# Kernel optimization log

Measured on AMD Instinct MI355X. Metric: run time of the kernel, lower is better.

The kernel has to match this reference:

```python
import jax, jax.numpy as jnp
import numpy as np

N = 20000   # nodes per type (lnc and dis)
E = 160000  # edges per meta-path graph and per pos/neg link graph
H = 8       # attention heads
D = 32      # out_size per head (H*D = 256 flattened)
HID = 256   # hidden_size from ResNet projection


def _bn(x, g, b, eps=1e-5):
    # training-mode BatchNorm1d (biased variance, like torch)
    m = x.mean(0)
    v = x.var(0)
    return g * (x - m) * jax.lax.rsqrt(v + eps) + b


def _leaky(x, slope):
    return jnp.where(x >= 0, x, slope * x)


def _gat(h_src, h_dst, src, dst, W, al, ar, n_dst):
    # DGL GATConv (bipartite, shared fc, no bias, eval mode)
    fs = (h_src @ W).reshape(-1, H, D)          # [Ns,H,D]
    fd = (h_dst @ W).reshape(-1, H, D)          # [Nd,H,D]
    el = (fs * al).sum(-1)                      # [Ns,H]
    er = (fd * ar).sum(-1)                      # [Nd,H]
    e = _leaky(el[src] + er[dst], 0.2)          # [E,H]
    emax = jax.ops.segment_max(e, dst, num_segments=n_dst)
    emax = jnp.where(jnp.isfinite(emax), emax, 0.0)   # zero in-degree safety
    ee = jnp.exp(e - emax[dst])
    den = jax.ops.segment_sum(ee, dst, num_segments=n_dst)
    a = ee / jnp.maximum(den[dst], 1e-9)        # edge softmax over incoming edges
    out = jax.ops.segment_sum(a[:, :, None] * fs[src], dst, num_segments=n_dst)
    return _leaky(out, 0.01).reshape(n_dst, H * D)  # activation=F.leaky_relu, flatten(1)


def _sem_attn(z, W1, b1, w2):
    # z: [N, 2, H*D]; SemanticAttention
    w = (jnp.tanh(z @ W1 + b1) @ w2).mean(0)    # [2]
    beta = jax.nn.softmax(w, axis=0)            # [2]
    return (beta[None, :, None] * z).sum(1)     # [N, H*D]


def setup_inputs() -> dict:
    key = jax.random.key(0)
    ks = jax.random.split(key, 32)
    s = 0.05
    inp = {
        "x_lnc": jax.random.normal(ks[0], (N, 256), jnp.float32),
        "x_dis": jax.random.normal(ks[1], (N, 256), jnp.float32),
        "proj_W": jax.random.normal(ks[2], (2, 256, HID), jnp.float32) * s,
        "proj_bn_g": jnp.ones((HID,), jnp.float32),
        "proj_bn_b": jnp.zeros((HID,), jnp.float32),
        "short_W": jax.random.normal(ks[3], (2, 256, HID), jnp.float32) * s,
        "short_b": jnp.zeros((2, HID), jnp.float32),
        "gat_W": jax.random.normal(ks[4], (4, HID, H * D), jnp.float32) * s,
        "gat_al": jax.random.normal(ks[5], (4, H, D), jnp.float32) * s,
        "gat_ar": jax.random.normal(ks[6], (4, H, D), jnp.float32) * s,
        "sem_W1": jax.random.normal(ks[7], (H * D, 128), jnp.float32) * s,
        "sem_b1": jnp.zeros((128,), jnp.float32),
        "sem_w2": jax.random.normal(ks[8], (128,), jnp.float32) * s,
    }
    names = ["ld_src", "ld_dst", "ll_src", "ll_dst", "dl_src", "dl_dst",
             "dd_src", "dd_dst", "pos_src", "pos_dst", "neg_src", "neg_dst"]
    for i, nm in enumerate(names):
        inp[nm] = jax.random.randint(ks[10 + i], (E,), 0, N, jnp.int32)
    return inp


def reference(x_lnc, x_dis, proj_W, proj_bn_g, proj_bn_b, short_W, short_b,
              gat_W, gat_al, gat_ar, sem_W1, sem_b1, sem_w2,
              ld_src, ld_dst, ll_src, ll_dst, dl_src, dl_dst,
              dd_src, dd_dst, pos_src, pos_dst, neg_src, neg_dst):
    # ResNet projection (shared BN applied per-branch, training-mode stats)
    l_x = _leaky(_bn(x_lnc @ proj_W[0], proj_bn_g, proj_bn_b), 0.01) + (x_lnc @ short_W[0] + short_b[0])
    d_x = _leaky(_bn(x_dis @ proj_W[1], proj_bn_g, proj_bn_b), 0.01) + (x_dis @ short_W[1] + short_b[1])
    # HANLayer: 4 meta-path GATs with pairings (l,d),(l,l),(d,l),(d,d)
    e0 = _gat(l_x, d_x, ld_src, ld_dst, gat_W[0], gat_al[0], gat_ar[0], N)  # dst dis
    e1 = _gat(l_x, l_x, ll_src, ll_dst, gat_W[1], gat_al[1], gat_ar[1], N)  # dst lnc
    e2 = _gat(d_x, l_x, dl_src, dl_dst, gat_W[2], gat_al[2], gat_ar[2], N)  # dst lnc
    e3 = _gat(d_x, d_x, dd_src, dd_dst, gat_W[3], gat_al[3], gat_ar[3], N)  # dst dis
    l_embs = _sem_attn(jnp.stack((e1, e2), axis=1), sem_W1, sem_b1, sem_w2)
    d_embs = _sem_attn(jnp.stack((e0, e3), axis=1), sem_W1, sem_b1, sem_w2)
    # Hadamard u_mul_v over 'lnc-dis' edges (pos graph and neg graph)
    pos_z = l_embs[pos_src] * d_embs[pos_dst]
    neg_z = l_embs[neg_src] * d_embs[neg_dst]
    return pos_z, neg_z, l_embs, d_embs
```

## Files before the change

### kernel.cpp

```cpp
#include <hip/hip_runtime.h>
#include <math.h>

#define NN 20000
#define NE 160000
#define SLOT 40

typedef _Float16 f16;
typedef __attribute__((ext_vector_type(8))) _Float16 f16x8;
typedef __attribute__((ext_vector_type(4))) float f32x4;

__device__ __forceinline__ float leakyf(float x, float s){ return x >= 0.f ? x : s*x; }
__device__ __forceinline__ ushort f2h(float x){ f16 h = (f16)x; ushort u; __builtin_memcpy(&u,&h,2); return u; }
__device__ __forceinline__ float h2f(ushort u){ f16 h; __builtin_memcpy(&h,&u,2); return (float)h; }

__device__ __forceinline__ void gload_lds16(const void* g, void* l){
  __builtin_amdgcn_global_load_lds((const __attribute__((address_space(1))) uint*)g,
                                   (__attribute__((address_space(3))) uint*)l, 16, 0, 0);
}
__device__ __forceinline__ void nts4(float* p, f32x4 v){
  __builtin_nontemporal_store(v, (f32x4*)p);
}

__global__ __launch_bounds__(256) void prep(const float* __restrict__ x_lnc,
    const float* __restrict__ x_dis, const float* __restrict__ proj_W,
    const float* __restrict__ short_W, const float* __restrict__ gat_W,
    const float* __restrict__ gat_al, const float* __restrict__ gat_ar,
    const float* __restrict__ sem_W1,
    ushort* __restrict__ xhl, ushort* __restrict__ xhd,
    ushort* btpl, ushort* btpd, ushort* btgl, ushort* btgd, ushort* btsm,
    int* __restrict__ zbuf){
  int b = blockIdx.x;
  if (b < 10000){
    const float* in = (b >= 5000) ? x_dis : x_lnc;
    ushort* out = (b >= 5000) ? xhd : xhl;
    long idx = (long)(b % 5000)*256 + threadIdx.x;
    long r = idx>>6; int c4 = (int)(idx&63)<<2;
    float4 v = *(const float4*)(in + r*256 + c4);
    ushort4 o; o.x=f2h(v.x); o.y=f2h(v.y); o.z=f2h(v.z); o.w=f2h(v.w);
    *(ushort4*)(out + r*256 + c4) = o;
  } else if (b < 10168){
    int t = b - 10000;
    const float* S; ushort* outb; int n0, k0, ldS=256, colbase;
    if (t < 160){
      int m = t >> 4, tt = t & 15;
      n0 = (tt & 3) * 64; k0 = (tt >> 2) * 64;
      switch(m){
        case 0: S=proj_W;        outb=btpl; colbase=0;   break;
        case 1: S=short_W;       outb=btpl; colbase=256; break;
        case 2: S=proj_W+65536;  outb=btpd; colbase=0;   break;
        case 3: S=short_W+65536; outb=btpd; colbase=256; break;
        case 4: S=gat_W;         outb=btgl; colbase=0;   break;
        case 5: S=gat_W+65536;   outb=btgl; colbase=256; break;
        case 6: S=gat_W+131072;  outb=btgl; colbase=512; break;
        case 7: S=gat_W;         outb=btgd; colbase=0;   break;
        case 8: S=gat_W+131072;  outb=btgd; colbase=256; break;
        default:S=gat_W+196608;  outb=btgd; colbase=512; break;
      }
    } else {
      int s = t - 160;
      n0 = (s & 1)*64; k0 = (s >> 1)*64; ldS = 128;
      S = sem_W1; outb = btsm; colbase = 0;
    }
    __shared__ float tile[64][65];
    int tr = threadIdx.x >> 6;
    int tc = threadIdx.x & 63;
    #pragma unroll
    for (int p=0;p<16;p++){
      int kr = p*4 + tr;
      tile[kr][tc] = S[(size_t)(k0+kr)*ldS + n0 + tc];
    }
    __syncthreads();
    #pragma unroll
    for (int p=0;p<16;p++){
      int nr = p*4 + tr;
      outb[(size_t)(colbase + n0 + nr)*256 + k0 + tc] = f2h(tile[tc][nr]);
    }
  } else if (b < 10232){
    int idx = (b-10168)*256 + threadIdx.x;
    int side = idx >> 13;
    int r = idx & 8191;
    int c = r >> 8;
    int k = r & 255;
    int h = c & 7, sel = c >> 3;
    int gi; const float* av;
    if (side==0){
      gi = (sel==0)?0:((sel==3)?2:1);
      av = (sel<=1)? gat_al : gat_ar;
    } else {
      gi = (sel==0)?0:((sel==1)?2:3);
      av = (sel==1||sel==2)? gat_al : gat_ar;
    }
    const float* wrow = gat_W + gi*65536 + (size_t)k*256 + h*32;
    const float* a = av + gi*256 + h*32;
    float s = 0.f;
    #pragma unroll
    for (int d=0; d<32; d++) s += wrow[d]*a[d];
    ushort* out = side ? btgd : btgl;
    out[(size_t)(768+c)*256 + k] = f2h(s);
  } else if (b < 10328){
    int idx = (b-10232)*256 + threadIdx.x;
    uint* pl = (uint*)(btgl + 800*256);
    uint* pd = (uint*)(btgd + 800*256);
    if (idx < 12288) pl[idx] = 0; else pd[idx-12288] = 0;
  } else {
    int idx = (b-10328)*256 + threadIdx.x;
    if (idx < 81028) zbuf[idx] = 0;
  }
}

template<int EPI>
__global__ __launch_bounds__(256) void gemm16(
    const ushort* __restrict__ A0, const ushort* __restrict__ A1,
    const ushort* __restrict__ B0, const ushort* __restrict__ B1,
    ushort* __restrict__ C0, ushort* __restrict__ C1, int ldc, int M,
    float* __restrict__ sbuf,
    float* __restrict__ elr_l, float* __restrict__ elr_d,
    const float* __restrict__ b1v, const float* __restrict__ w2v,
    const int* s0, const int* s1, const int* s2, const int* s3,
    const int* d0, const int* d1, const int* d2, const int* d3,
    int* __restrict__ cnt, int* __restrict__ slots){
  const int z = blockIdx.z;
  if (EPI==1 && z==2){
    int bb = blockIdx.y*gridDim.x + blockIdx.x;
    int tid = bb*256 + (int)threadIdx.x;
    if (tid < NE){
      #pragma unroll
      for (int g=0; g<4; g++){
        const int* src = (g==0)?s0:(g==1)?s1:(g==2)?s2:s3;
        const int* dst = (g==0)?d0:(g==1)?d1:(g==2)?d2:d3;
        int d = dst[tid];
        int p = atomicAdd(&cnt[g*NN + d], 1);
        slots[(size_t)(g*NN + d)*SLOT + p] = src[tid];
      }
    }
    return;
  }
  int bx, by;
  {
    int gx = gridDim.x, gy = gridDim.y;
    int nwg = gx*gy;
    int bid = blockIdx.y*gx + blockIdx.x;
    int q = nwg>>3, r = nwg&7;
    int xcd = bid&7, ii = bid>>3;
    int swz = (xcd<r ? xcd*(q+1) : r*(q+1)+(xcd-r)*q) + ii;
    bx = swz % gx; by = swz / gx;
  }
  const ushort* A = z ? A1 : A0;
  const ushort* Bt = z ? B1 : B0;
  ushort* C = z ? C1 : C0;
  __shared__ ushort sm[16384];
  char* smc = (char*)sm;
  const int tid = threadIdx.x;
  const int lane = tid & 63, wid = tid >> 6;
  const int wr = wid >> 1, wc = wid & 1;
  const int fr = lane & 15, fq = lane >> 4;
  const int brow = by*128, bcol = bx*128;
  f32x4 acc[4][4];
  #pragma unroll
  for (int i=0;i<4;i++)
    #pragma unroll
    for (int j=0;j<4;j++) acc[i][j] = (f32x4){0.f,0.f,0.f,0.f};

  for (int k0 = 0; k0 < 256; k0 += 64){
    __syncthreads();
    #pragma unroll
    for (int cc = 0; cc < 8; cc++){
      int c = wid*8 + cc;
      int ch = c & 15;
      int rel = ch*1024 + lane*16;
      int row = rel >> 7;
      int scb = (rel & 127) ^ ((row & 7) << 4);
      const char* src;
      if (c < 16){
        int gr = brow + row; gr = (gr < M) ? gr : (M-1);
        src = (const char*)A + (size_t)gr*512 + k0*2 + scb;
      } else {
        src = (const char*)Bt + (size_t)(bcol + row)*512 + k0*2 + scb;
      }
      gload_lds16(src, smc + ((c<16)?0:16384) + ch*1024);
    }
    __syncthreads();
    #pragma unroll
    for (int ks = 0; ks < 2; ks++){
      f16x8 af[4], bfr[4];
      #pragma unroll
      for (int i=0;i<4;i++){
        int r = wr*64 + i*16 + fr;
        int koff = ks*32 + fq*8;
        int aoff = ((r<<7) + koff*2) ^ ((r&7)<<4);
        af[i] = *(const f16x8*)(smc + aoff);
        int n = wc*64 + i*16 + fr;
        int boff = ((n<<7) + koff*2) ^ ((n&7)<<4);
        bfr[i] = *(const f16x8*)(smc + 16384 + boff);
      }
      #pragma unroll
      for (int i=0;i<4;i++)
        #pragma unroll
        for (int j=0;j<4;j++)
          acc[i][j] = __builtin_amdgcn_mfma_f32_16x16x32_f16(af[i], bfr[j], acc[i][j], 0,0,0);
    }
  }

  if (EPI==1 || (EPI==2 && bcol < 768)){
    #pragma unroll
    for (int i=0;i<4;i++){
      #pragma unroll
      for (int e=0;e<4;e++){
        int gr = brow + wr*64 + i*16 + fq*4 + e;
        if (gr < M){
          #pragma unroll
          for (int j=0;j<4;j++)
            C[(size_t)gr*ldc + bcol + wc*64 + j*16 + fr] = f2h(acc[i][j][e]);
        }
      }
    }
  }

  if (EPI==2 && bcol >= 768 && wc == 0){
    float* elr = z ? elr_d : elr_l;
    #pragma unroll
    for (int i=0;i<4;i++){
      #pragma unroll
      for (int e=0;e<4;e++){
        int gr = brow + wr*64 + i*16 + fq*4 + e;
        if (gr < M){
          elr[(size_t)gr*32 + fr]      = acc[i][0][e];
          elr[(size_t)gr*32 + 16 + fr] = acc[i][1][e];
        }
      }
    }
  }

  if (EPI==1 && bcol < 256){
    float* gsum = sbuf + z*512;
    float* gsq  = gsum + 256;
    #pragma unroll
    for (int j=0;j<4;j++){
      float s=0.f, q=0.f;
      #pragma unroll
      for (int i=0;i<4;i++)
        #pragma unroll
        for (int e=0;e<4;e++){
          int gr = brow + wr*64 + i*16 + fq*4 + e;
          if (gr < M){ float v = acc[i][j][e]; s += v; q += v*v; }
        }
      s += __shfl_xor(s,16); s += __shfl_xor(s,32);
      q += __shfl_xor(q,16); q += __shfl_xor(q,32);
      if (fq==0){
        int gc = bcol + wc*64 + j*16 + fr;
        atomicAdd(&gsum[gc], s);
        atomicAdd(&gsq[gc], q);
      }
    }
  }

  if (EPI==3){
    float b1c[4], w2c[4];
    #pragma unroll
    for (int j=0;j<4;j++){
      int col = wc*64 + j*16 + fr;
      b1c[j] = b1v[col]; w2c[j] = w2v[col];
    }
    int segA = brow/20000;
    int bound = (segA+1)*20000;
    float t0=0.f, t1=0.f;
    #pragma unroll
    for (int i=0;i<4;i++){
      #pragma unroll
      for (int e=0;e<4;e++){
        int gr = brow + wr*64 + i*16 + fq*4 + e;
        float rs = 0.f;
        #pragma unroll
        for (int j=0;j<4;j++){
          float x = acc[i][j][e] + b1c[j];
          float ex = __expf(2.f*x);
          rs += (1.f - 2.f/(ex+1.f))*w2c[j];
        }
        if (gr < bound) t0 += rs; else t1 += rs;
      }
    }
    #pragma unroll
    for (int off=32; off>0; off>>=1){ t0 += __shfl_xor(t0,off); t1 += __shfl_xor(t1,off); }
    if (lane==0){
      atomicAdd(&sbuf[segA], t0);
      if (brow + 127 >= bound) atomicAdd(&sbuf[segA+1], t1);
    }
  }
}

__global__ __launch_bounds__(256) void proj_apply2(const ushort* __restrict__ PS_l,
    const ushort* __restrict__ PS_d, const float* __restrict__ sbuf,
    const float* __restrict__ gg, const float* __restrict__ bb,
    const float* __restrict__ short_b, ushort* __restrict__ out_l, ushort* __restrict__ out_d){
  int y = blockIdx.y;
  const ushort* PS = y ? PS_d : PS_l;
  ushort* out = y ? out_d : out_l;
  const float* gsum = sbuf + y*512;
  const float* gsq  = gsum + 256;
  const float* sb = short_b + y*256;
  long idx = (long)blockIdx.x*256 + threadIdx.x;
  long r = idx>>6; int c4 = (int)(idx&63)<<2;
  ushort4 pu = *(const ushort4*)(PS + r*512 + c4);
  ushort4 su = *(const ushort4*)(PS + r*512 + 256 + c4);
  float pv[4] = {h2f(pu.x),h2f(pu.y),h2f(pu.z),h2f(pu.w)};
  float sv[4] = {h2f(su.x),h2f(su.y),h2f(su.z),h2f(su.w)};
  ushort o[4];
  #pragma unroll
  for (int k=0;k<4;k++){
    int c = c4+k;
    float m = gsum[c]*(1.f/NN);
    float va = gsq[c]*(1.f/NN) - m*m;
    float ri = rsqrtf(va + 1e-5f);
    float yv = (pv[k]-m)*ri*gg[c] + bb[c];
    o[k] = f2h(leakyf(yv,0.01f) + sv[k] + sb[c]);
  }
  ushort4 ov; ov.x=o[0]; ov.y=o[1]; ov.z=o[2]; ov.w=o[3];
  *(ushort4*)(out + r*256 + c4) = ov;
}

__global__ __launch_bounds__(256) void gat_fused(const int* __restrict__ cnt,
    const int* __restrict__ slots, const float* __restrict__ elr_l,
    const float* __restrict__ elr_d, const ushort* __restrict__ fc_l,
    const ushort* __restrict__ fc_d, ushort* __restrict__ sems){
  const int g = blockIdx.y;
  const int n = blockIdx.x*4 + (threadIdx.x>>6);
  const int lane = threadIdx.x & 63;
  const int co[4]    = {0,256,256,512};
  const int semo[4]  = {40000,0,20000,60000};
  const int eloA[4]  = {0,8,8,16};
  const int eroA[4]  = {0,16,24,24};
  const float* elb = (g<2) ? elr_l : elr_d;
  const float* erb = (g==1||g==2) ? elr_l : elr_d;
  const int eloff = eloA[g], eroff = eroA[g];
  const ushort* F = (g<2) ? fc_l : fc_d;
  const int coloff = co[g];
  const int j = lane>>3, h = lane&7, hc = lane>>3;
  const int e1 = cnt[g*NN + n];
  const long sb = (long)(g*NN + n)*SLOT;
  const float ern = erb[(size_t)n*32 + eroff + h];
  float ssum = 0.f;
  float4 acc = make_float4(0.f,0.f,0.f,0.f);

  for (int base = 0; base < e1; base += 8){
    int idx = base + j;
    bool valid = idx < e1;
    int src = valid ? slots[sb + idx] : 0;
    float p = valid ? __expf(leakyf(elb[(size_t)src*32 + eloff + h] + ern, 0.2f)) : 0.f;
    ssum += p;
    #pragma unroll
    for (int e=0;e<8;e++){
      float w = __shfl(p, e*8 + hc);
      int s = __shfl(src, e*8);
      ushort4 fu = *(const ushort4*)(F + (size_t)s*768 + coloff + lane*4);
      acc.x = fmaf(w,h2f(fu.x),acc.x); acc.y = fmaf(w,h2f(fu.y),acc.y);
      acc.z = fmaf(w,h2f(fu.z),acc.z); acc.w = fmaf(w,h2f(fu.w),acc.w);
    }
  }
  ssum += __shfl_xor(ssum,8); ssum += __shfl_xor(ssum,16); ssum += __shfl_xor(ssum,32);
  float rd = 1.f/fmaxf(__shfl(ssum, hc), 1e-9f);
  ushort4 o;
  o.x = f2h(leakyf(acc.x*rd, 0.01f)); o.y = f2h(leakyf(acc.y*rd, 0.01f));
  o.z = f2h(leakyf(acc.z*rd, 0.01f)); o.w = f2h(leakyf(acc.w*rd, 0.01f));
  *(ushort4*)(sems + (size_t)(semo[g]+n)*256 + lane*4) = o;
}

__global__ __launch_bounds__(256) void sem_combine(const ushort* __restrict__ sems,
    const float* __restrict__ tsum, float* __restrict__ lemb, float* __restrict__ demb,
    ushort* __restrict__ lemb16, ushort* __restrict__ demb16){
  float wl0 = tsum[0]*(1.f/20000.f), wl1 = tsum[1]*(1.f/20000.f);
  float m = fmaxf(wl0,wl1);
  float ea = __expf(wl0-m), eb = __expf(wl1-m);
  float b0 = ea/(ea+eb), b1 = eb/(ea+eb);
  float wd0 = tsum[2]*(1.f/20000.f), wd1 = tsum[3]*(1.f/20000.f);
  m = fmaxf(wd0,wd1);
  ea = __expf(wd0-m); eb = __expf(wd1-m);
  float b2 = ea/(ea+eb), b3 = eb/(ea+eb);

  long idx = (long)blockIdx.x*256 + threadIdx.x;
  long r = idx>>6; int c4 = (int)(idx&63)<<2;
  ushort4 v1 = *(const ushort4*)(sems + (r          )*256 + c4);
  ushort4 v2 = *(const ushort4*)(sems + (r + 20000L )*256 + c4);
  ushort4 v0 = *(const ushort4*)(sems + (r + 40000L )*256 + c4);
  ushort4 v3 = *(const ushort4*)(sems + (r + 60000L )*256 + c4);
  f32x4 lo, dd;
  lo[0] = b0*h2f(v1.x) + b1*h2f(v2.x); dd[0] = b2*h2f(v0.x) + b3*h2f(v3.x);
  lo[1] = b0*h2f(v1.y) + b1*h2f(v2.y); dd[1] = b2*h2f(v0.y) + b3*h2f(v3.y);
  lo[2] = b0*h2f(v1.z) + b1*h2f(v2.z); dd[2] = b2*h2f(v0.z) + b3*h2f(v3.z);
  lo[3] = b0*h2f(v1.w) + b1*h2f(v2.w); dd[3] = b2*h2f(v0.w) + b3*h2f(v3.w);
  nts4(lemb + r*256 + c4, lo);
  nts4(demb + r*256 + c4, dd);
  ushort4 lh, dh;
  lh.x=f2h(lo[0]); lh.y=f2h(lo[1]); lh.z=f2h(lo[2]); lh.w=f2h(lo[3]);
  dh.x=f2h(dd[0]); dh.y=f2h(dd[1]); dh.z=f2h(dd[2]); dh.w=f2h(dd[3]);
  *(ushort4*)(lemb16 + r*256 + c4) = lh;
  *(ushort4*)(demb16 + r*256 + c4) = dh;
}

__global__ __launch_bounds__(256) void edge_mul2(const int* __restrict__ ps, const int* __restrict__ pd,
    const int* __restrict__ ns, const int* __restrict__ nd,
    const ushort* __restrict__ lemb16, const ushort* __restrict__ demb16,
    float* __restrict__ pos, float* __restrict__ neg){
  long idx = (long)blockIdx.x*256 + threadIdx.x;
  const long H = (long)NE*32;
  const int *es, *ed; float* out; long t;
  if (idx < H){ es=ps; ed=pd; out=pos; t=idx; }
  else { es=ns; ed=nd; out=neg; t=idx-H; }
  long i = t>>5; int jj = (int)(t&31);
  int s = es[i], d = ed[i];
  f16x8 a = *(const f16x8*)(lemb16 + (size_t)s*256 + (size_t)jj*8);
  f16x8 b = *(const f16x8*)(demb16 + (size_t)d*256 + (size_t)jj*8);
  f32x4 o0, o1;
  o0[0]=(float)a[0]*(float)b[0]; o0[1]=(float)a[1]*(float)b[1];
  o0[2]=(float)a[2]*(float)b[2]; o0[3]=(float)a[3]*(float)b[3];
  o1[0]=(float)a[4]*(float)b[4]; o1[1]=(float)a[5]*(float)b[5];
  o1[2]=(float)a[6]*(float)b[6]; o1[3]=(float)a[7]*(float)b[7];
  float* op = out + (size_t)i*256 + (size_t)jj*8;
  nts4(op, o0);
  nts4(op+4, o1);
}

extern "C" void kernel_launch(void* const* d_in, const int* in_sizes, int n_in,
                              void* d_out, int out_size, void* d_ws, size_t ws_size,
                              hipStream_t stream){
  const float* x_lnc  = (const float*)d_in[0];
  const float* x_dis  = (const float*)d_in[1];
  const float* proj_W = (const float*)d_in[2];
  const float* bn_g   = (const float*)d_in[3];
  const float* bn_b   = (const float*)d_in[4];
  const float* short_W= (const float*)d_in[5];
  const float* short_b= (const float*)d_in[6];
  const float* gat_W  = (const float*)d_in[7];
  const float* gat_al = (const float*)d_in[8];
  const float* gat_ar = (const float*)d_in[9];
  const float* sem_W1 = (const float*)d_in[10];
  const float* sem_b1 = (const float*)d_in[11];
  const float* sem_w2 = (const float*)d_in[12];
  const int* g_src[4] = {(const int*)d_in[13],(const int*)d_in[15],(const int*)d_in[17],(const int*)d_in[19]};
  const int* g_dst[4] = {(const int*)d_in[14],(const int*)d_in[16],(const int*)d_in[18],(const int*)d_in[20]};
  const int* pos_src = (const int*)d_in[21];
  const int* pos_dst = (const int*)d_in[22];
  const int* neg_src = (const int*)d_in[23];
  const int* neg_dst = (const int*)d_in[24];

  const long LEMB = (long)NN*256;
  const long EOUT = (long)NE*256;

  float* outf = (float*)d_out;
  float* pos  = outf;
  float* negr = outf + EOUT;
  float* lemb = outf + 2*EOUT;
  float* demb = lemb + LEMB;

  ushort* PS_l = (ushort*)negr;
  ushort* PS_d = PS_l + 10240000;
  ushort* fc_l = (ushort*)negr;
  ushort* fc_d = fc_l + 15360000;

  float* ws   = (float*)d_ws;
  float* sbuf = ws;
  float* tsum = ws + 1024;
  int*   cnt  = (int*)(ws + 1028);
  float* elr_l = ws + 81028;
  float* elr_d = elr_l + 640000;
  int*   slots  = (int*)(elr_d + 640000);
  ushort* xhl  = (ushort*)(slots + 3200000);
  ushort* xhd  = xhl + 5120000;
  ushort* axl  = xhd + 5120000;
  ushort* axd  = axl + 5120000;
  ushort* sems = axd + 5120000;
  ushort* lemb16 = sems + 20480000;
  ushort* demb16 = lemb16 + 5120000;
  ushort* btpl = demb16 + 5120000;
  ushort* btpd = btpl + 131072;
  ushort* btgl = btpd + 131072;
  ushort* btgd = btgl + 229376;
  ushort* btsm = btgd + 229376;

  prep<<<10645,256,0,stream>>>(x_lnc, x_dis, proj_W, short_W, gat_W, gat_al, gat_ar,
                               sem_W1, xhl, xhd, btpl, btpd, btgl, btgd, btsm, (int*)ws);

  gemm16<1><<<dim3(4,157,3),256,0,stream>>>(xhl, xhd, btpl, btpd, PS_l, PS_d, 512, NN,
      sbuf, nullptr, nullptr, nullptr, nullptr,
      g_src[0],g_src[1],g_src[2],g_src[3], g_dst[0],g_dst[1],g_dst[2],g_dst[3],
      cnt, slots);
  proj_apply2<<<dim3(5000,2),256,0,stream>>>(PS_l, PS_d, sbuf, bn_g, bn_b, short_b, axl, axd);

  gemm16<2><<<dim3(7,157,2),256,0,stream>>>(axl, axd, btgl, btgd, fc_l, fc_d, 768, NN,
      nullptr, elr_l, elr_d, nullptr, nullptr,
      nullptr,nullptr,nullptr,nullptr, nullptr,nullptr,nullptr,nullptr, nullptr,nullptr);

  gat_fused<<<dim3(5000,4),256,0,stream>>>(cnt, slots, elr_l, elr_d, fc_l, fc_d, sems);

  gemm16<3><<<dim3(1,625,1),256,0,stream>>>(sems, nullptr, btsm, nullptr, nullptr, nullptr, 128, 80000,
      tsum, nullptr, nullptr, sem_b1, sem_w2,
      nullptr,nullptr,nullptr,nullptr, nullptr,nullptr,nullptr,nullptr, nullptr,nullptr);

  sem_combine<<<5000,256,0,stream>>>(sems, tsum, lemb, demb, lemb16, demb16);

  edge_mul2<<<40000,256,0,stream>>>(pos_src, pos_dst, neg_src, neg_dst, lemb16, demb16, pos, negr);
}
```

Before: 364.1 us.

## Fuse fp32-to-fp16 input conversion into projection GEMM A-tile loads

Removes the separate conversion pass in prep that wrote fp16 copies of x_lnc and x_dis. The EPI==1 GEMM now reads fp32 rows directly, converts them to fp16 in registers and writes the swizzled tile into LDS. This saves a full read/write round trip of both inputs and shrinks the prep launch. It also drops the XCD-aware block swizzle for all GEMMs, which may change L2 locality, and replaces the async global_load_lds path for A with ordinary loads and LDS stores that read twice as many bytes.

```diff
diff --git a/kernel.cpp b/kernel.cpp
--- a/kernel.cpp
+++ b/kernel.cpp
@@ -21,25 +21,15 @@
   __builtin_nontemporal_store(v, (f32x4*)p);
 }
 
-__global__ __launch_bounds__(256) void prep(const float* __restrict__ x_lnc,
-    const float* __restrict__ x_dis, const float* __restrict__ proj_W,
+__global__ __launch_bounds__(256) void prep(const float* __restrict__ proj_W,
     const float* __restrict__ short_W, const float* __restrict__ gat_W,
     const float* __restrict__ gat_al, const float* __restrict__ gat_ar,
     const float* __restrict__ sem_W1,
-    ushort* __restrict__ xhl, ushort* __restrict__ xhd,
     ushort* btpl, ushort* btpd, ushort* btgl, ushort* btgd, ushort* btsm,
     int* __restrict__ zbuf){
   int b = blockIdx.x;
-  if (b < 10000){
-    const float* in = (b >= 5000) ? x_dis : x_lnc;
-    ushort* out = (b >= 5000) ? xhd : xhl;
-    long idx = (long)(b % 5000)*256 + threadIdx.x;
-    long r = idx>>6; int c4 = (int)(idx&63)<<2;
-    float4 v = *(const float4*)(in + r*256 + c4);
-    ushort4 o; o.x=f2h(v.x); o.y=f2h(v.y); o.z=f2h(v.z); o.w=f2h(v.w);
-    *(ushort4*)(out + r*256 + c4) = o;
-  } else if (b < 10168){
-    int t = b - 10000;
+  if (b < 168){
+    int t = b;
     const float* S; ushort* outb; int n0, k0, ldS=256, colbase;
     if (t < 160){
       int m = t >> 4, tt = t & 15;
@@ -75,8 +65,8 @@
       int nr = p*4 + tr;
       outb[(size_t)(colbase + n0 + nr)*256 + k0 + tc] = f2h(tile[tc][nr]);
     }
-  } else if (b < 10232){
-    int idx = (b-10168)*256 + threadIdx.x;
+  } else if (b < 232){
+    int idx = (b-168)*256 + threadIdx.x;
     int side = idx >> 13;
     int r = idx & 8191;
     int c = r >> 8;
@@ -97,19 +87,20 @@
     for (int d=0; d<32; d++) s += wrow[d]*a[d];
     ushort* out = side ? btgd : btgl;
     out[(size_t)(768+c)*256 + k] = f2h(s);
-  } else if (b < 10328){
-    int idx = (b-10232)*256 + threadIdx.x;
+  } else if (b < 328){
+    int idx = (b-232)*256 + threadIdx.x;
     uint* pl = (uint*)(btgl + 800*256);
     uint* pd = (uint*)(btgd + 800*256);
     if (idx < 12288) pl[idx] = 0; else pd[idx-12288] = 0;
   } else {
-    int idx = (b-10328)*256 + threadIdx.x;
+    int idx = (b-328)*256 + threadIdx.x;
     if (idx < 81028) zbuf[idx] = 0;
   }
 }
 
 template<int EPI>
 __global__ __launch_bounds__(256) void gemm16(
+    const float* __restrict__ Af0, const float* __restrict__ Af1,
     const ushort* __restrict__ A0, const ushort* __restrict__ A1,
     const ushort* __restrict__ B0, const ushort* __restrict__ B1,
     ushort* __restrict__ C0, ushort* __restrict__ C1, int ldc, int M,
@@ -135,16 +126,7 @@
     }
     return;
   }
-  int bx, by;
-  {
-    int gx = gridDim.x, gy = gridDim.y;
-    int nwg = gx*gy;
-    int bid = blockIdx.y*gx + blockIdx.x;
-    int q = nwg>>3, r = nwg&7;
-    int xcd = bid&7, ii = bid>>3;
-    int swz = (xcd<r ? xcd*(q+1) : r*(q+1)+(xcd-r)*q) + ii;
-    bx = swz % gx; by = swz / gx;
-  }
+  const float* Af = z ? Af1 : Af0;
   const ushort* A = z ? A1 : A0;
   const ushort* Bt = z ? B1 : B0;
   ushort* C = z ? C1 : C0;
@@ -154,7 +136,7 @@
   const int lane = tid & 63, wid = tid >> 6;
   const int wr = wid >> 1, wc = wid & 1;
   const int fr = lane & 15, fq = lane >> 4;
-  const int brow = by*128, bcol = bx*128;
+  const int brow = blockIdx.y*128, bcol = blockIdx.x*128;
   f32x4 acc[4][4];
   #pragma unroll
   for (int i=0;i<4;i++)
@@ -169,15 +151,26 @@
       int ch = c & 15;
       int rel = ch*1024 + lane*16;
       int row = rel >> 7;
-      int scb = (rel & 127) ^ ((row & 7) << 4);
-      const char* src;
+      int colb = rel & 127;
+      int scb = colb ^ ((row & 7) << 4);
       if (c < 16){
         int gr = brow + row; gr = (gr < M) ? gr : (M-1);
-        src = (const char*)A + (size_t)gr*512 + k0*2 + scb;
+        if (EPI==1){
+          const float* srcf = Af + (size_t)gr*256 + k0 + (colb>>1);
+          float4 v0 = *(const float4*)(srcf);
+          float4 v1 = *(const float4*)(srcf + 4);
+          f16x8 hv;
+          hv[0]=(f16)v0.x; hv[1]=(f16)v0.y; hv[2]=(f16)v0.z; hv[3]=(f16)v0.w;
+          hv[4]=(f16)v1.x; hv[5]=(f16)v1.y; hv[6]=(f16)v1.z; hv[7]=(f16)v1.w;
+          *(f16x8*)(smc + (rel & ~127) + scb) = hv;
+        } else {
+          const char* src = (const char*)A + (size_t)gr*512 + k0*2 + scb;
+          gload_lds16(src, smc + ch*1024);
+        }
       } else {
-        src = (const char*)Bt + (size_t)(bcol + row)*512 + k0*2 + scb;
-      }
-      gload_lds16(src, smc + ((c<16)?0:16384) + ch*1024);
+        const char* src = (const char*)Bt + (size_t)(bcol + row)*512 + k0*2 + scb;
+        gload_lds16(src, smc + 16384 + ch*1024);
+      }
     }
     __syncthreads();
     #pragma unroll
@@ -463,9 +456,7 @@
   float* elr_l = ws + 81028;
   float* elr_d = elr_l + 640000;
   int*   slots  = (int*)(elr_d + 640000);
-  ushort* xhl  = (ushort*)(slots + 3200000);
-  ushort* xhd  = xhl + 5120000;
-  ushort* axl  = xhd + 5120000;
+  ushort* axl  = (ushort*)(slots + 3200000);
   ushort* axd  = axl + 5120000;
   ushort* sems = axd + 5120000;
   ushort* lemb16 = sems + 20480000;
@@ -476,22 +467,25 @@
   ushort* btgd = btgl + 229376;
   ushort* btsm = btgd + 229376;
 
-  prep<<<10645,256,0,stream>>>(x_lnc, x_dis, proj_W, short_W, gat_W, gat_al, gat_ar,
-                               sem_W1, xhl, xhd, btpl, btpd, btgl, btgd, btsm, (int*)ws);
-
-  gemm16<1><<<dim3(4,157,3),256,0,stream>>>(xhl, xhd, btpl, btpd, PS_l, PS_d, 512, NN,
+  prep<<<645,256,0,stream>>>(proj_W, short_W, gat_W, gat_al, gat_ar,
+                             sem_W1, btpl, btpd, btgl, btgd, btsm, (int*)ws);
+
+  gemm16<1><<<dim3(4,157,3),256,0,stream>>>(x_lnc, x_dis, nullptr, nullptr,
+      btpl, btpd, PS_l, PS_d, 512, NN,
       sbuf, nullptr, nullptr, nullptr, nullptr,
       g_src[0],g_src[1],g_src[2],g_src[3], g_dst[0],g_dst[1],g_dst[2],g_dst[3],
       cnt, slots);
   proj_apply2<<<dim3(5000,2),256,0,stream>>>(PS_l, PS_d, sbuf, bn_g, bn_b, short_b, axl, axd);
 
-  gemm16<2><<<dim3(7,157,2),256,0,stream>>>(axl, axd, btgl, btgd, fc_l, fc_d, 768, NN,
+  gemm16<2><<<dim3(7,157,2),256,0,stream>>>(nullptr, nullptr, axl, axd,
+      btgl, btgd, fc_l, fc_d, 768, NN,
       nullptr, elr_l, elr_d, nullptr, nullptr,
       nullptr,nullptr,nullptr,nullptr, nullptr,nullptr,nullptr,nullptr, nullptr,nullptr);
 
   gat_fused<<<dim3(5000,4),256,0,stream>>>(cnt, slots, elr_l, elr_d, fc_l, fc_d, sems);
 
-  gemm16<3><<<dim3(1,625,1),256,0,stream>>>(sems, nullptr, btsm, nullptr, nullptr, nullptr, 128, 80000,
+  gemm16<3><<<dim3(1,625,1),256,0,stream>>>(nullptr, nullptr, sems, nullptr,
+      btsm, nullptr, nullptr, nullptr, 128, 80000,
       tsum, nullptr, nullptr, sem_b1, sem_w2,
       nullptr,nullptr,nullptr,nullptr, nullptr,nullptr,nullptr,nullptr, nullptr,nullptr);
 
```

Measured after the change: 390.5 us. 1.07x slower.
